# Kernel tuning notes

Hardware: AMD Instinct MI355X
Metric: run time of the kernel (lower is better)

Reference implementation:

```python
import jax, jax.numpy as jnp
import numpy as np

B, S, D = 4, 2048, 512
H, DK, DV = 8, 64, 64
DFF = 2048
LN_EPS = 1e-5


def _layernorm(x, g, b):
    mu = jnp.mean(x, axis=-1, keepdims=True)
    var = jnp.mean(jnp.square(x - mu), axis=-1, keepdims=True)
    return (x - mu) * jax.lax.rsqrt(var + LN_EPS) * g + b


def setup_inputs() -> dict:
    key = jax.random.key(0)
    ks = jax.random.split(key, 9)
    def xavier(k, shape):
        fan_out, fan_in = shape
        std = np.sqrt(2.0 / (fan_in + fan_out))
        return jax.random.normal(k, shape, jnp.float32) * std
    GELU_GAIN = 1.85
    return {
        "x": jax.random.normal(ks[0], (B, S, D), jnp.float32),
        "attention_mask": jax.random.randint(ks[1], (B, S), 0, 2).astype(bool),
        "Wq": xavier(ks[2], (H * DK, D)),
        "Wk": xavier(ks[3], (H * DK, D)),
        "Wv": xavier(ks[4], (H * DV, D)),
        "Wp": xavier(ks[5], (D, H * DV)),
        "W1": xavier(ks[6], (DFF, D)) * GELU_GAIN,
        "b1": jnp.zeros((DFF,), jnp.float32),
        "W2": xavier(ks[7], (D, DFF)),
        "b2": jnp.zeros((D,), jnp.float32),
        "ln1_g": jnp.ones((D,), jnp.float32),
        "ln1_b": jnp.zeros((D,), jnp.float32),
        "ln2_g": jnp.ones((D,), jnp.float32),
        "ln2_b": jnp.zeros((D,), jnp.float32),
    }


def reference(x, attention_mask, Wq, Wk, Wv, Wp, W1, b1, W2, b2,
              ln1_g, ln1_b, ln2_g, ln2_b):
    b, s, d = x.shape
    residual = x
    q = (x @ Wq.T).reshape(b, s, H, DK)  # [B,S,H,DK]
    k = (x @ Wk.T).reshape(b, s, H, DK)
    v = (x @ Wv.T).reshape(b, s, H, DV)
    score = jnp.einsum("bshd,bthd->bhst", q, k) * (DK ** -0.5)  # [B,H,S,S]
    # subtractive mask: score -= 100 * not(mask)
    score = score - 100.0 * (~attention_mask)[:, None, None, :].astype(score.dtype)
    p = jax.nn.softmax(score, axis=-1)
    ctx = jnp.einsum("bhst,bthd->bshd", p, v).reshape(b, s, H * DV)
    att = ctx @ Wp.T  # dropout p=0.1 is identity in eval
    h = _layernorm(att + residual, ln1_g, ln1_b)
    ff = jax.nn.gelu(h @ W1.T + b1, approximate=False) @ W2.T + b2
    out = _layernorm(ff + h, ln2_g, ln2_b)
    return out
```

## Files before the change

kernel.cpp:

```cpp
#include <hip/hip_runtime.h>
#include <cstdint>
#include <cstddef>

#define B_ 4
#define S_ 2048
#define D_ 512
#define H_ 8
#define DK_ 64
#define DFF_ 2048

using s16x8  = __attribute__((ext_vector_type(8))) short;
using bf16x8 = __attribute__((ext_vector_type(8))) __bf16;
using f32x4  = __attribute__((ext_vector_type(4))) float;

__device__ __forceinline__ short f2bf(float f) {
  unsigned u = __builtin_bit_cast(unsigned, f);
  u += 0x7FFFu + ((u >> 16) & 1u);
  return (short)(u >> 16);
}
__device__ __forceinline__ float bf2f(short s) {
  unsigned u = ((unsigned)(unsigned short)s) << 16;
  return __builtin_bit_cast(float, u);
}

__device__ __forceinline__ void gl2lds16(const void* g, void* l) {
  __builtin_amdgcn_global_load_lds(
      (const __attribute__((address_space(1))) void*)g,
      (__attribute__((address_space(3))) void*)l, 16, 0, 0);
}

__global__ __launch_bounds__(256)
void cvt_all(const float* __restrict__ x, const float* __restrict__ Wq,
             const float* __restrict__ Wk, const float* __restrict__ Wv,
             const float* __restrict__ Wp, const float* __restrict__ W1,
             const float* __restrict__ W2,
             short* __restrict__ xb, short* __restrict__ wqkv,
             short* __restrict__ wp, short* __restrict__ w1, short* __restrict__ w2) {
  int blk = blockIdx.x;
  const float* src; short* dst; int off;
  if (blk < 4096)      { src = x;  dst = xb;            off = blk; }
  else if (blk < 4352) { src = Wq; dst = wqkv;          off = blk - 4096; }
  else if (blk < 4608) { src = Wk; dst = wqkv + 262144; off = blk - 4352; }
  else if (blk < 4864) { src = Wv; dst = wqkv + 524288; off = blk - 4608; }
  else if (blk < 5120) { src = Wp; dst = wp;            off = blk - 4864; }
  else if (blk < 6144) { src = W1; dst = w1;            off = blk - 5120; }
  else                 { src = W2; dst = w2;            off = blk - 6144; }
  int i = (off * 256 + threadIdx.x) * 4;
  float4 v = *(const float4*)(src + i);
  *(short4*)(dst + i) = make_short4(f2bf(v.x), f2bf(v.y), f2bf(v.z), f2bf(v.w));
}

template <int MODE>
__global__ __launch_bounds__(256)
void gemm_bt(const short* __restrict__ A, const short* __restrict__ B,
             int M, int N, int K,
             const float* __restrict__ aux1,
             void* __restrict__ out0, void* __restrict__ out1, void* __restrict__ out2) {
  __shared__ alignas(16) short As[128][64];
  __shared__ alignas(16) short Bs[128][64];

  const int tid  = threadIdx.x;
  const int lane = tid & 63;
  const int wave = tid >> 6;
  const int quad = lane >> 4;
  const int l16  = lane & 15;
  const int wm   = (wave >> 1) * 64;
  const int wn   = (wave & 1) * 64;
  const int bm   = blockIdx.x * 128;
  const int bn   = blockIdx.y * 128;
  const int Kh   = K / gridDim.z;
  const int koff = blockIdx.z * Kh;

  const int srow8 = lane >> 3;
  const int pb    = lane & 7;

  f32x4 acc[4][4] = {};

  for (int k0 = 0; k0 < Kh; k0 += 64) {
#pragma unroll
    for (int i = 0; i < 4; ++i) {
      const int rr = wave * 32 + i * 8 + srow8;
      const int cb = pb ^ (rr & 7);
      gl2lds16(A + (size_t)(bm + rr) * K + koff + k0 + cb * 8, &As[wave * 32 + i * 8][0]);
      gl2lds16(B + (size_t)(bn + rr) * K + koff + k0 + cb * 8, &Bs[wave * 32 + i * 8][0]);
    }
    __syncthreads();

#pragma unroll
    for (int c = 0; c < 2; ++c) {
      bf16x8 a[4], b[4];
#pragma unroll
      for (int i = 0; i < 4; ++i) {
        const int row = wm + i * 16 + l16;
        const int pba = (c * 4 + quad) ^ (row & 7);
        a[i] = __builtin_bit_cast(bf16x8, *(const s16x8*)&As[row][pba * 8]);
      }
#pragma unroll
      for (int j = 0; j < 4; ++j) {
        const int row = wn + j * 16 + l16;
        const int pbb = (c * 4 + quad) ^ (row & 7);
        b[j] = __builtin_bit_cast(bf16x8, *(const s16x8*)&Bs[row][pbb * 8]);
      }
#pragma unroll
      for (int i = 0; i < 4; ++i)
#pragma unroll
        for (int j = 0; j < 4; ++j)
          acc[i][j] = __builtin_amdgcn_mfma_f32_16x16x32_bf16(a[i], b[j], acc[i][j], 0, 0, 0);
    }
    __syncthreads();
  }

#pragma unroll
  for (int i = 0; i < 4; ++i) {
    const int m0 = bm + wm + i * 16 + quad * 4;
#pragma unroll
    for (int j = 0; j < 4; ++j) {
      const int n = bn + wn + j * 16 + l16;
      if constexpr (MODE == 0) {
        const int bb = m0 >> 11, ss0 = m0 & 2047;
        if (n < 512) {
          short4 pk = make_short4(f2bf(acc[i][j][0] * 0.18033688f), f2bf(acc[i][j][1] * 0.18033688f),
                                  f2bf(acc[i][j][2] * 0.18033688f), f2bf(acc[i][j][3] * 0.18033688f));
          *(short4*)((short*)out0 +
              ((((size_t)bb * H_ + (n >> 6)) * 64 + (n & 63)) * S_ + ss0)) = pk;
        } else if (n >= 1024) {
          const int nn = n - 1024;
          short4 pk = make_short4(f2bf(acc[i][j][0]), f2bf(acc[i][j][1]),
                                  f2bf(acc[i][j][2]), f2bf(acc[i][j][3]));
          *(short4*)((short*)out2 +
              ((((size_t)bb * H_ + (nn >> 6)) * 64 + (nn & 63)) * S_ + ss0)) = pk;
        } else {
          const int nn = n - 512;
          const size_t rowb = ((size_t)bb * H_ + (nn >> 6)) * S_ + ss0;
#pragma unroll
          for (int rr = 0; rr < 4; ++rr)
            ((short*)out1)[(rowb + rr) * 64 + (nn & 63)] = f2bf(acc[i][j][rr]);
        }
      } else if constexpr (MODE == 1) {
        float* dst = (float*)out0 + (size_t)blockIdx.z * M * N;
#pragma unroll
        for (int rr = 0; rr < 4; ++rr)
          dst[(size_t)(m0 + rr) * N + n] = acc[i][j][rr];
      } else {
#pragma unroll
        for (int rr = 0; rr < 4; ++rr) {
          float t = acc[i][j][rr] + aux1[n];
          float x2 = t * t;
          float t2 = t * (2.3022082f + 0.1029464f * x2);
          float e  = __builtin_amdgcn_exp2f(t2);
          float gl = t - t * __builtin_amdgcn_rcpf(1.0f + e);
          ((short*)out0)[(size_t)(m0 + rr) * N + n] = f2bf(gl);
        }
      }
    }
  }
}

__global__ __launch_bounds__(256)
void flash_attn_mfma(const short* __restrict__ QTg, const short* __restrict__ Kb,
                     const short* __restrict__ Vtg, const void* __restrict__ mraw,
                     short* __restrict__ ctxb) {
  __shared__ alignas(16) short Ks[64][64];
  __shared__ alignas(16) short Vt[64][64];
  __shared__ alignas(16) short Ps[4][32][64];
  __shared__ alignas(8) unsigned char mbits8[256];
  __shared__ unsigned red[4];

  int flat = (blockIdx.z * 8 + blockIdx.y) * 16 + blockIdx.x;
  flat = (flat & 7) * 64 + (flat >> 3);
  const int b = flat >> 7, h = (flat >> 4) & 7;
  const int q0 = (flat & 15) * 128;

  const int tid = threadIdx.x;
  const int w = tid >> 6, lane = tid & 63;
  const int quad = lane >> 4, l16 = lane & 15;
  const size_t base  = ((size_t)(b * H_ + h)) * S_ * DK_;
  const size_t baseT = ((size_t)(b * H_ + h)) * DK_ * S_;

  {
    const unsigned* mw = (const unsigned*)mraw;
    unsigned v = 0;
#pragma unroll
    for (int i = 0; i < 8; ++i) v |= mw[tid + i * 256];
#pragma unroll
    for (int s = 1; s < 64; s <<= 1) v |= __shfl_xor(v, s);
    if (lane == 0) red[w] = v;
    __syncthreads();
    unsigned f = red[0] | red[1] | red[2] | red[3];
    unsigned byte = 0;
#pragma unroll
    for (int j = 0; j < 8; ++j) {
      int t = tid * 8 + j;
      int gidx = b * S_ + t;
      int val;
      if ((f & ~1u) == 0u)            val = ((const int*)mraw)[gidx];
      else if (f == 0x3F800000u)      val = (((const float*)mraw)[gidx] != 0.0f);
      else                            val = ((const unsigned char*)mraw)[gidx];
      byte |= (val ? 1u : 0u) << j;
    }
    mbits8[tid] = (unsigned char)byte;
  }

  bf16x8 qa[2][2];
#pragma unroll
  for (int st = 0; st < 2; ++st) {
    const int q = q0 + w * 32 + st * 16 + l16;
#pragma unroll
    for (int c = 0; c < 2; ++c) {
      s16x8 t;
#pragma unroll
      for (int j = 0; j < 8; ++j)
        t[j] = QTg[baseT + (size_t)(c * 32 + quad * 8 + j) * S_ + q];
      qa[st][c] = __builtin_bit_cast(bf16x8, t);
    }
  }

  f32x4 Oc[2][4] = {};
  float li[2] = {};
  const int swz = l16 & 7;

  const int r = tid >> 2, cc = tid & 3;
  const short* kp = Kb  + base  + (size_t)r * 64 + cc * 16;
  const short* vp = Vtg + baseT + (size_t)r * S_ + cc * 16;
  const int ch0 = (((cc * 2)     ^ (r & 7)) << 3);
  const int ch1 = (((cc * 2 + 1) ^ (r & 7)) << 3);

  s16x8 kr0 = *(const s16x8*)(kp);
  s16x8 kr1 = *(const s16x8*)(kp + 8);
  s16x8 vr0 = *(const s16x8*)(vp);
  s16x8 vr1 = *(const s16x8*)(vp + 8);

  for (int t0 = 0; t0 < S_; t0 += 64) {
    __syncthreads();
    *(s16x8*)&Ks[r][ch0] = kr0;
    *(s16x8*)&Ks[r][ch1] = kr1;
    *(s16x8*)&Vt[r][ch0] = vr0;
    *(s16x8*)&Vt[r][ch1] = vr1;
    __syncthreads();

    if (t0 + 64 < S_) {
      kr0 = *(const s16x8*)(kp + (size_t)(t0 + 64) * 64);
      kr1 = *(const s16x8*)(kp + (size_t)(t0 + 64) * 64 + 8);
      vr0 = *(const s16x8*)(vp + (t0 + 64));
      vr1 = *(const s16x8*)(vp + (t0 + 64) + 8);
    }

    f32x4 sc[2][4] = {};
    __builtin_amdgcn_s_setprio(1);
#pragma unroll
    for (int c = 0; c < 2; ++c) {
#pragma unroll
      for (int jt = 0; jt < 4; ++jt) {
        bf16x8 kb = __builtin_bit_cast(bf16x8,
            *(const s16x8*)&Ks[jt * 16 + l16][((c * 4 + quad) ^ swz) << 3]);
        sc[0][jt] = __builtin_amdgcn_mfma_f32_16x16x32_bf16(kb, qa[0][c], sc[0][jt], 0, 0, 0);
        sc[1][jt] = __builtin_amdgcn_mfma_f32_16x16x32_bf16(kb, qa[1][c], sc[1][jt], 0, 0, 0);
      }
    }
    __builtin_amdgcn_s_setprio(0);

    const unsigned long long mball =
        *(const unsigned long long*)&mbits8[t0 >> 3];
#pragma unroll
    for (int jt = 0; jt < 4; ++jt) {
      const unsigned m16 = ((unsigned)(mball >> (jt * 16))) >> (quad * 4);
      const int pch = (((jt * 2 + (quad >> 1)) ^ swz) << 3) + (quad & 1) * 4;
#pragma unroll
      for (int st = 0; st < 2; ++st) {
        unsigned uu[4];
#pragma unroll
        for (int rr = 0; rr < 4; ++rr) {
          float pe = __builtin_amdgcn_exp2f(sc[st][jt][rr]);
          unsigned u = __builtin_bit_cast(unsigned, pe) & 0xFFFF0000u;
          u = ((m16 >> rr) & 1u) ? u : 0u;
          li[st] += __builtin_bit_cast(float, u);
          uu[rr] = u;
        }
        *(uint2*)&Ps[w][st * 16 + l16][pch] =
            make_uint2(__builtin_amdgcn_perm(uu[1], uu[0], 0x07060302u),
                       __builtin_amdgcn_perm(uu[3], uu[2], 0x07060302u));
      }
    }

    __builtin_amdgcn_s_setprio(1);
#pragma unroll
    for (int c = 0; c < 2; ++c) {
      bf16x8 pa0 = __builtin_bit_cast(bf16x8,
          *(const s16x8*)&Ps[w][l16][((c * 4 + quad) ^ swz) << 3]);
      bf16x8 pa1 = __builtin_bit_cast(bf16x8,
          *(const s16x8*)&Ps[w][16 + l16][((c * 4 + quad) ^ swz) << 3]);
#pragma unroll
      for (int dt = 0; dt < 4; ++dt) {
        bf16x8 vb = __builtin_bit_cast(bf16x8,
            *(const s16x8*)&Vt[dt * 16 + l16][((c * 4 + quad) ^ swz) << 3]);
        Oc[0][dt] = __builtin_amdgcn_mfma_f32_16x16x32_bf16(pa0, vb, Oc[0][dt], 0, 0, 0);
        Oc[1][dt] = __builtin_amdgcn_mfma_f32_16x16x32_bf16(pa1, vb, Oc[1][dt], 0, 0, 0);
      }
    }
    __builtin_amdgcn_s_setprio(0);
  }

#pragma unroll
  for (int st = 0; st < 2; ++st) {
    float l = li[st];
    l += __shfl_xor(l, 16);
    l += __shfl_xor(l, 32);
#pragma unroll
    for (int rr = 0; rr < 4; ++rr) {
      float lr = __shfl(l, quad * 4 + rr);
      float inv = 1.f / lr;
      const size_t row = (size_t)b * S_ + q0 + w * 32 + st * 16 + quad * 4 + rr;
#pragma unroll
      for (int dt = 0; dt < 4; ++dt)
        ctxb[row * (H_ * DK_) + h * 64 + dt * 16 + l16] = f2bf(Oc[st][dt][rr] * inv);
    }
  }
}

__global__ __launch_bounds__(256)
void ln_fused(const float* __restrict__ p0, const float* __restrict__ p1,
              const float* __restrict__ xres, const short* __restrict__ hres,
              const float* __restrict__ bias,
              const float* __restrict__ g, const float* __restrict__ bb,
              float* __restrict__ out32, short* __restrict__ outb) {
  const int wave = threadIdx.x >> 6, lane = threadIdx.x & 63;
  const int token = blockIdx.x * 4 + wave;
  const size_t off = (size_t)token * D_;
  const int c = lane * 8;

  float v[8];
  {
    float4 a0 = *(const float4*)(p0 + off + c);
    float4 a1 = *(const float4*)(p0 + off + c + 4);
    float4 b0 = *(const float4*)(p1 + off + c);
    float4 b1 = *(const float4*)(p1 + off + c + 4);
    v[0]=a0.x+b0.x; v[1]=a0.y+b0.y; v[2]=a0.z+b0.z; v[3]=a0.w+b0.w;
    v[4]=a1.x+b1.x; v[5]=a1.y+b1.y; v[6]=a1.z+b1.z; v[7]=a1.w+b1.w;
  }
  if (xres) {
    float4 x0 = *(const float4*)(xres + off + c);
    float4 x1 = *(const float4*)(xres + off + c + 4);
    v[0]+=x0.x; v[1]+=x0.y; v[2]+=x0.z; v[3]+=x0.w;
    v[4]+=x1.x; v[5]+=x1.y; v[6]+=x1.z; v[7]+=x1.w;
  }
  if (hres) {
    short4 h0 = *(const short4*)(hres + off + c);
    short4 h1 = *(const short4*)(hres + off + c + 4);
    v[0]+=bf2f(h0.x); v[1]+=bf2f(h0.y); v[2]+=bf2f(h0.z); v[3]+=bf2f(h0.w);
    v[4]+=bf2f(h1.x); v[5]+=bf2f(h1.y); v[6]+=bf2f(h1.z); v[7]+=bf2f(h1.w);
  }
  if (bias) {
    float4 c0 = *(const float4*)(bias + c);
    float4 c1 = *(const float4*)(bias + c + 4);
    v[0]+=c0.x; v[1]+=c0.y; v[2]+=c0.z; v[3]+=c0.w;
    v[4]+=c1.x; v[5]+=c1.y; v[6]+=c1.z; v[7]+=c1.w;
  }

  float sum = 0.f;
#pragma unroll
  for (int i = 0; i < 8; ++i) sum += v[i];
#pragma unroll
  for (int m = 1; m < 64; m <<= 1) sum += __shfl_xor(sum, m);
  float mu = sum * (1.0f / D_);
  float vs = 0.f;
#pragma unroll
  for (int i = 0; i < 8; ++i) { v[i] -= mu; vs += v[i] * v[i]; }
#pragma unroll
  for (int m = 1; m < 64; m <<= 1) vs += __shfl_xor(vs, m);
  float rstd = rsqrtf(vs * (1.0f / D_) + 1e-5f);
#pragma unroll
  for (int i = 0; i < 8; ++i) {
    float val = v[i] * rstd * g[c + i] + bb[c + i];
    if (out32) out32[off + c + i] = val;
    if (outb)  outb[off + c + i] = f2bf(val);
  }
}

constexpr size_t OFF_XB   = 0;
constexpr size_t OFF_WQKV = 8388608;
constexpr size_t OFF_WP   = 9961472;
constexpr size_t OFF_W1   = 10485760;
constexpr size_t OFF_W2   = 12582912;
constexpr size_t OFF_QT   = 14680064;
constexpr size_t OFF_K    = 23068672;
constexpr size_t OFF_VT   = 31457280;
constexpr size_t OFF_CTX  = 39845888;
constexpr size_t OFF_P0   = 48234496;
constexpr size_t OFF_P1   = 65011712;
constexpr size_t OFF_HB   = 81788928;
constexpr size_t OFF_FF1  = 14680064;
constexpr size_t WS_NEED  = 90177536;

extern "C" void kernel_launch(void* const* d_in, const int* in_sizes, int n_in,
                              void* d_out, int out_size, void* d_ws, size_t ws_size,
                              hipStream_t stream) {
  if (ws_size < WS_NEED) return;

  const float* x    = (const float*)d_in[0];
  const void*  msk  = d_in[1];
  const float* Wq   = (const float*)d_in[2];
  const float* Wk   = (const float*)d_in[3];
  const float* Wv   = (const float*)d_in[4];
  const float* Wp   = (const float*)d_in[5];
  const float* W1   = (const float*)d_in[6];
  const float* b1   = (const float*)d_in[7];
  const float* W2   = (const float*)d_in[8];
  const float* b2   = (const float*)d_in[9];
  const float* ln1g = (const float*)d_in[10];
  const float* ln1b = (const float*)d_in[11];
  const float* ln2g = (const float*)d_in[12];
  const float* ln2b = (const float*)d_in[13];

  char* ws = (char*)d_ws;
  short* xb    = (short*)(ws + OFF_XB);
  short* wqkv  = (short*)(ws + OFF_WQKV);
  short* Wpb   = (short*)(ws + OFF_WP);
  short* W1b   = (short*)(ws + OFF_W1);
  short* W2b   = (short*)(ws + OFF_W2);
  short* QTb   = (short*)(ws + OFF_QT);
  short* Kbh   = (short*)(ws + OFF_K);
  short* VTb   = (short*)(ws + OFF_VT);
  short* ctxb  = (short*)(ws + OFF_CTX);
  float* p0    = (float*)(ws + OFF_P0);
  short* hb    = (short*)(ws + OFF_HB);
  short* ff1b  = (short*)(ws + OFF_FF1);

  cvt_all<<<7168, 256, 0, stream>>>(x, Wq, Wk, Wv, Wp, W1, W2,
                                    xb, wqkv, Wpb, W1b, W2b);

  gemm_bt<0><<<dim3(64, 12, 1), 256, 0, stream>>>(xb, wqkv, 8192, 1536, 512,
                                                  nullptr, QTb, Kbh, VTb);

  flash_attn_mfma<<<dim3(S_ / 128, H_, B_), 256, 0, stream>>>(QTb, Kbh, VTb, msk, ctxb);

  gemm_bt<1><<<dim3(64, 4, 2), 256, 0, stream>>>(ctxb, Wpb, 8192, 512, 512,
                                                 nullptr, p0, nullptr, nullptr);

  ln_fused<<<2048, 256, 0, stream>>>(p0, p0 + (size_t)8192 * 512, x, nullptr, nullptr,
                                     ln1g, ln1b, nullptr, hb);

  gemm_bt<2><<<dim3(64, 16, 1), 256, 0, stream>>>(hb, W1b, 8192, 2048, 512,
                                                  b1, ff1b, nullptr, nullptr);

  gemm_bt<1><<<dim3(64, 4, 2), 256, 0, stream>>>(ff1b, W2b, 8192, 512, 2048,
                                                 nullptr, p0, nullptr, nullptr);

  ln_fused<<<2048, 256, 0, stream>>>(p0, p0 + (size_t)8192 * 512, nullptr, hb, b2,
                                     ln2g, ln2b, (float*)d_out, nullptr);
}
```

Baseline: 293.2 us.

## Split flash attention work across 8 waves with 16 query rows each

Doubles the attention block from 4 to 8 waves, so each wave handles 16 query rows instead of 32, and each thread loads one 16-byte chunk of K and V per tile instead of two. The goal is more waves per block to hide latency and spread the exp and MFMA work, with fewer registers per thread. In exchange, each K/V tile loaded into shared memory is reused by half as many query rows per wave, there are more MFMA-issuing waves contending, and barrier cost per tile rises with the larger block.

```diff
diff --git a/kernel.cpp b/kernel.cpp
--- a/kernel.cpp
+++ b/kernel.cpp
@@ -156,15 +156,15 @@
   }
 }
 
-__global__ __launch_bounds__(256)
+__global__ __launch_bounds__(512)
 void flash_attn_mfma(const short* __restrict__ QTg, const short* __restrict__ Kb,
                      const short* __restrict__ Vtg, const void* __restrict__ mraw,
                      short* __restrict__ ctxb) {
   __shared__ alignas(16) short Ks[64][64];
   __shared__ alignas(16) short Vt[64][64];
-  __shared__ alignas(16) short Ps[4][32][64];
+  __shared__ alignas(16) short Ps[8][16][64];
   __shared__ alignas(8) unsigned char mbits8[256];
-  __shared__ unsigned red[4];
+  __shared__ unsigned red[8];
 
   int flat = (blockIdx.z * 8 + blockIdx.y) * 16 + blockIdx.x;
   flat = (flat & 7) * 64 + (flat >> 3);
@@ -181,71 +181,66 @@
     const unsigned* mw = (const unsigned*)mraw;
     unsigned v = 0;
 #pragma unroll
-    for (int i = 0; i < 8; ++i) v |= mw[tid + i * 256];
+    for (int i = 0; i < 4; ++i) v |= mw[tid + i * 512];
 #pragma unroll
     for (int s = 1; s < 64; s <<= 1) v |= __shfl_xor(v, s);
     if (lane == 0) red[w] = v;
     __syncthreads();
-    unsigned f = red[0] | red[1] | red[2] | red[3];
-    unsigned byte = 0;
-#pragma unroll
-    for (int j = 0; j < 8; ++j) {
-      int t = tid * 8 + j;
-      int gidx = b * S_ + t;
-      int val;
-      if ((f & ~1u) == 0u)            val = ((const int*)mraw)[gidx];
-      else if (f == 0x3F800000u)      val = (((const float*)mraw)[gidx] != 0.0f);
-      else                            val = ((const unsigned char*)mraw)[gidx];
-      byte |= (val ? 1u : 0u) << j;
-    }
-    mbits8[tid] = (unsigned char)byte;
-  }
-
-  bf16x8 qa[2][2];
-#pragma unroll
-  for (int st = 0; st < 2; ++st) {
-    const int q = q0 + w * 32 + st * 16 + l16;
+    unsigned f = red[0] | red[1] | red[2] | red[3] |
+                 red[4] | red[5] | red[6] | red[7];
+    if (tid < 256) {
+      unsigned byte = 0;
+#pragma unroll
+      for (int j = 0; j < 8; ++j) {
+        int t = tid * 8 + j;
+        int gidx = b * S_ + t;
+        int val;
+        if ((f & ~1u) == 0u)            val = ((const int*)mraw)[gidx];
+        else if (f == 0x3F800000u)      val = (((const float*)mraw)[gidx] != 0.0f);
+        else                            val = ((const unsigned char*)mraw)[gidx];
+        byte |= (val ? 1u : 0u) << j;
+      }
+      mbits8[tid] = (unsigned char)byte;
+    }
+  }
+
+  bf16x8 qa[2];
+  {
+    const int q = q0 + w * 16 + l16;
 #pragma unroll
     for (int c = 0; c < 2; ++c) {
       s16x8 t;
 #pragma unroll
       for (int j = 0; j < 8; ++j)
         t[j] = QTg[baseT + (size_t)(c * 32 + quad * 8 + j) * S_ + q];
-      qa[st][c] = __builtin_bit_cast(bf16x8, t);
-    }
-  }
-
-  f32x4 Oc[2][4] = {};
-  float li[2] = {};
+      qa[c] = __builtin_bit_cast(bf16x8, t);
+    }
+  }
+
+  f32x4 Oc[4] = {};
+  float li = 0.f;
   const int swz = l16 & 7;
 
-  const int r = tid >> 2, cc = tid & 3;
-  const short* kp = Kb  + base  + (size_t)r * 64 + cc * 16;
-  const short* vp = Vtg + baseT + (size_t)r * S_ + cc * 16;
-  const int ch0 = (((cc * 2)     ^ (r & 7)) << 3);
-  const int ch1 = (((cc * 2 + 1) ^ (r & 7)) << 3);
-
-  s16x8 kr0 = *(const s16x8*)(kp);
-  s16x8 kr1 = *(const s16x8*)(kp + 8);
-  s16x8 vr0 = *(const s16x8*)(vp);
-  s16x8 vr1 = *(const s16x8*)(vp + 8);
+  const int r = tid >> 3, cc = tid & 7;
+  const short* kp = Kb  + base  + (size_t)r * 64 + cc * 8;
+  const short* vp = Vtg + baseT + (size_t)r * S_ + cc * 8;
+  const int ch = ((cc ^ (r & 7)) << 3);
+
+  s16x8 kr = *(const s16x8*)(kp);
+  s16x8 vr = *(const s16x8*)(vp);
 
   for (int t0 = 0; t0 < S_; t0 += 64) {
     __syncthreads();
-    *(s16x8*)&Ks[r][ch0] = kr0;
-    *(s16x8*)&Ks[r][ch1] = kr1;
-    *(s16x8*)&Vt[r][ch0] = vr0;
-    *(s16x8*)&Vt[r][ch1] = vr1;
+    *(s16x8*)&Ks[r][ch] = kr;
+    *(s16x8*)&Vt[r][ch] = vr;
     __syncthreads();
 
     if (t0 + 64 < S_) {
-      kr0 = *(const s16x8*)(kp + (size_t)(t0 + 64) * 64);
-      kr1 = *(const s16x8*)(kp + (size_t)(t0 + 64) * 64 + 8);
-      vr0 = *(const s16x8*)(vp + (t0 + 64));
-      vr1 = *(const s16x8*)(vp + (t0 + 64) + 8);
-    }
-
-    f32x4 sc[2][4] = {};
+      kr = *(const s16x8*)(kp + (size_t)(t0 + 64) * 64);
+      vr = *(const s16x8*)(vp + (t0 + 64));
+    }
+
+    f32x4 sc[4] = {};
     __builtin_amdgcn_s_setprio(1);
 #pragma unroll
     for (int c = 0; c < 2; ++c) {
@@ -253,8 +248,7 @@
       for (int jt = 0; jt < 4; ++jt) {
         bf16x8 kb = __builtin_bit_cast(bf16x8,
             *(const s16x8*)&Ks[jt * 16 + l16][((c * 4 + quad) ^ swz) << 3]);
-        sc[0][jt] = __builtin_amdgcn_mfma_f32_16x16x32_bf16(kb, qa[0][c], sc[0][jt], 0, 0, 0);
-        sc[1][jt] = __builtin_amdgcn_mfma_f32_16x16x32_bf16(kb, qa[1][c], sc[1][jt], 0, 0, 0);
+        sc[jt] = __builtin_amdgcn_mfma_f32_16x16x32_bf16(kb, qa[c], sc[jt], 0, 0, 0);
       }
     }
     __builtin_amdgcn_s_setprio(0);
@@ -265,54 +259,47 @@
     for (int jt = 0; jt < 4; ++jt) {
       const unsigned m16 = ((unsigned)(mball >> (jt * 16))) >> (quad * 4);
       const int pch = (((jt * 2 + (quad >> 1)) ^ swz) << 3) + (quad & 1) * 4;
-#pragma unroll
-      for (int st = 0; st < 2; ++st) {
-        unsigned uu[4];
-#pragma unroll
-        for (int rr = 0; rr < 4; ++rr) {
-          float pe = __builtin_amdgcn_exp2f(sc[st][jt][rr]);
-          unsigned u = __builtin_bit_cast(unsigned, pe) & 0xFFFF0000u;
-          u = ((m16 >> rr) & 1u) ? u : 0u;
-          li[st] += __builtin_bit_cast(float, u);
-          uu[rr] = u;
-        }
-        *(uint2*)&Ps[w][st * 16 + l16][pch] =
-            make_uint2(__builtin_amdgcn_perm(uu[1], uu[0], 0x07060302u),
-                       __builtin_amdgcn_perm(uu[3], uu[2], 0x07060302u));
-      }
+      unsigned uu[4];
+#pragma unroll
+      for (int rr = 0; rr < 4; ++rr) {
+        float pe = __builtin_amdgcn_exp2f(sc[jt][rr]);
+        unsigned u = __builtin_bit_cast(unsigned, pe) & 0xFFFF0000u;
+        u = ((m16 >> rr) & 1u) ? u : 0u;
+        li += __builtin_bit_cast(float, u);
+        uu[rr] = u;
+      }
+      *(uint2*)&Ps[w][l16][pch] =
+          make_uint2(__builtin_amdgcn_perm(uu[1], uu[0], 0x07060302u),
+                     __builtin_amdgcn_perm(uu[3], uu[2], 0x07060302u));
     }
 
     __builtin_amdgcn_s_setprio(1);
 #pragma unroll
     for (int c = 0; c < 2; ++c) {
-      bf16x8 pa0 = __builtin_bit_cast(bf16x8,
+      bf16x8 pa = __builtin_bit_cast(bf16x8,
           *(const s16x8*)&Ps[w][l16][((c * 4 + quad) ^ swz) << 3]);
-      bf16x8 pa1 = __builtin_bit_cast(bf16x8,
-          *(const s16x8*)&Ps[w][16 + l16][((c * 4 + quad) ^ swz) << 3]);
 #pragma unroll
       for (int dt = 0; dt < 4; ++dt) {
         bf16x8 vb = __builtin_bit_cast(bf16x8,
             *(const s16x8*)&Vt[dt * 16 + l16][((c * 4 + quad) ^ swz) << 3]);
-        Oc[0][dt] = __builtin_amdgcn_mfma_f32_16x16x32_bf16(pa0, vb, Oc[0][dt], 0, 0, 0);
-        Oc[1][dt] = __builtin_amdgcn_mfma_f32_16x16x32_bf16(pa1, vb, Oc[1][dt], 0, 0, 0);
+        Oc[dt] = __builtin_amdgcn_mfma_f32_16x16x32_bf16(pa, vb, Oc[dt], 0, 0, 0);
       }
     }
     __builtin_amdgcn_s_setprio(0);
   }
 
-#pragma unroll
-  for (int st = 0; st < 2; ++st) {
-    float l = li[st];
+  {
+    float l = li;
     l += __shfl_xor(l, 16);
     l += __shfl_xor(l, 32);
 #pragma unroll
     for (int rr = 0; rr < 4; ++rr) {
       float lr = __shfl(l, quad * 4 + rr);
       float inv = 1.f / lr;
-      const size_t row = (size_t)b * S_ + q0 + w * 32 + st * 16 + quad * 4 + rr;
+      const size_t row = (size_t)b * S_ + q0 + w * 16 + quad * 4 + rr;
 #pragma unroll
       for (int dt = 0; dt < 4; ++dt)
-        ctxb[row * (H_ * DK_) + h * 64 + dt * 16 + l16] = f2bf(Oc[st][dt][rr] * inv);
+        ctxb[row * (H_ * DK_) + h * 64 + dt * 16 + l16] = f2bf(Oc[dt][rr] * inv);
     }
   }
 }
@@ -431,7 +418,7 @@
   gemm_bt<0><<<dim3(64, 12, 1), 256, 0, stream>>>(xb, wqkv, 8192, 1536, 512,
                                                   nullptr, QTb, Kbh, VTb);
 
-  flash_attn_mfma<<<dim3(S_ / 128, H_, B_), 256, 0, stream>>>(QTb, Kbh, VTb, msk, ctxb);
+  flash_attn_mfma<<<dim3(S_ / 128, H_, B_), 512, 0, stream>>>(QTb, Kbh, VTb, msk, ctxb);
 
   gemm_bt<1><<<dim3(64, 4, 2), 256, 0, stream>>>(ctxb, Wpb, 8192, 512, 512,
                                                  nullptr, p0, nullptr, nullptr);
```

Result: faster. 286.3 us (-2.4%).
